# Kernel optimization log

Hardware: AMD Instinct MI355X
Metric: run time of the kernel (lower is better)

Reference implementation:

```python
import jax, jax.numpy as jnp
import numpy as np
import math

B, T, H, W = 32, 256, 16, 16
NE, NH, NL = 768, 12, 8
DH = NE // NH
SEQ_LEN = 1024


def _ln(x, g, b, eps=1e-5):
    m = jnp.mean(x, axis=-1, keepdims=True)
    v = jnp.mean((x - m) ** 2, axis=-1, keepdims=True)
    return (x - m) * jax.lax.rsqrt(v + eps) * g + b


def setup_inputs() -> dict:
    key = jax.random.key(0)
    ks = jax.random.split(key, 24)
    s = 0.02
    d = {}
    d["img_feat"] = jax.random.normal(ks[0], (B, 2048, H, W), jnp.float32)
    d["vm_patches"] = jax.random.normal(ks[1], (B, T, 256), jnp.float32)
    d["fm_patches"] = jax.random.normal(ks[2], (B, T, 256), jnp.float32)
    # token embedding params
    d["conv_w"] = jax.random.normal(ks[3], (NE // 2, 2048, 3, 3), jnp.float32) * s
    d["conv_b"] = jnp.zeros((NE // 2,), jnp.float32)
    d["vm_w"] = jax.random.normal(ks[4], (256, NE // 4), jnp.float32) * s
    d["vm_b"] = jnp.zeros((NE // 4,), jnp.float32)
    d["fm_w"] = jax.random.normal(ks[5], (256, NE // 4), jnp.float32) * s
    d["fm_b"] = jnp.zeros((NE // 4,), jnp.float32)
    d["pos_emb"] = jax.random.normal(ks[6], (SEQ_LEN, NE), jnp.float32) * s
    # stacked per-layer block params (leading dim NL, consumed by lax.scan)
    d["ln1_g"] = jnp.ones((NL, NE), jnp.float32)
    d["ln1_b"] = jnp.zeros((NL, NE), jnp.float32)
    d["Wq"] = jax.random.normal(ks[7], (NL, NE, NE), jnp.float32) * s
    d["bq"] = jnp.zeros((NL, NE), jnp.float32)
    d["Wk"] = jax.random.normal(ks[8], (NL, NE, NE), jnp.float32) * s
    d["bk"] = jnp.zeros((NL, NE), jnp.float32)
    d["Wv"] = jax.random.normal(ks[9], (NL, NE, NE), jnp.float32) * s
    d["bv"] = jnp.zeros((NL, NE), jnp.float32)
    d["Wo"] = jax.random.normal(ks[10], (NL, NE, NE), jnp.float32) * s
    d["bo"] = jnp.zeros((NL, NE), jnp.float32)
    d["ln2_g"] = jnp.ones((NL, NE), jnp.float32)
    d["ln2_b"] = jnp.zeros((NL, NE), jnp.float32)
    d["W1"] = jax.random.normal(ks[11], (NL, NE, 4 * NE), jnp.float32) * s
    d["b1"] = jnp.zeros((NL, 4 * NE), jnp.float32)
    d["W2"] = jax.random.normal(ks[12], (NL, 4 * NE, NE), jnp.float32) * s
    d["b2"] = jnp.zeros((NL, NE), jnp.float32)
    # prediction head params
    d["dec_ln1_g"] = jnp.ones((NE,), jnp.float32)
    d["dec_ln1_b"] = jnp.zeros((NE,), jnp.float32)
    d["dec_w"] = jax.random.normal(ks[13], (NE, NE), jnp.float32) * s
    d["dec_b"] = jnp.zeros((NE,), jnp.float32)
    d["dec_ln2_g"] = jnp.ones((NE,), jnp.float32)
    d["dec_ln2_b"] = jnp.zeros((NE,), jnp.float32)
    d["head_w"] = jax.random.normal(ks[14], (NE, 256), jnp.float32) * s
    d["head_b"] = jnp.zeros((256,), jnp.float32)
    return d


def reference(img_feat, vm_patches, fm_patches, conv_w, conv_b, vm_w, vm_b, fm_w, fm_b,
              pos_emb, ln1_g, ln1_b, Wq, bq, Wk, bk, Wv, bv, Wo, bo, ln2_g, ln2_b,
              W1, b1, W2, b2, dec_ln1_g, dec_ln1_b, dec_w, dec_b, dec_ln2_g, dec_ln2_b,
              head_w, head_b):
    # conv token embed: [B,2048,H,W] -> [B, NE//2, H, W] -> [B, T, NE//2]
    i_emb = jax.lax.conv_general_dilated(
        img_feat, conv_w, (1, 1), "SAME",
        dimension_numbers=("NCHW", "OIHW", "NCHW")) + conv_b[None, :, None, None]
    i_emb = i_emb.reshape(B, NE // 2, T).transpose(0, 2, 1)
    vm_emb = vm_patches @ vm_w + vm_b  # [B,T,NE//4]
    fm_emb = fm_patches @ fm_w + fm_b  # [B,T,NE//4]
    x = jnp.concatenate([i_emb, vm_emb, fm_emb], axis=2) + pos_emb[:T][None]  # [B,T,NE]

    scale = 1.0 / math.sqrt(DH)

    def block(x, p):
        g1, bb1_, wq, bq_, wk, bk_, wv, bv_, wo, bo_, g2, bb2_, w1, bm1, w2, bm2 = p
        h = _ln(x, g1, bb1_)
        q = (h @ wq + bq_).reshape(B, T, NH, DH)
        k = (h @ wk + bk_).reshape(B, T, NH, DH)
        v = (h @ wv + bv_).reshape(B, T, NH, DH)
        # mask in the original forward is hard-coded all-ones -> no masking
        att = jax.nn.softmax(jnp.einsum('bthd,bshd->bhts', q, k) * scale, axis=-1)
        y = jnp.einsum('bhts,bshd->bthd', att, v).reshape(B, T, NE)
        x = x + y @ wo + bo_
        h2 = _ln(x, g2, bb2_)
        x = x + jax.nn.gelu(h2 @ w1 + bm1, approximate=False) @ w2 + bm2
        return x, None

    x, _ = jax.lax.scan(block, x, (ln1_g, ln1_b, Wq, bq, Wk, bk, Wv, bv, Wo, bo,
                                   ln2_g, ln2_b, W1, b1, W2, b2))

    # Transformer_Prediction head
    x = _ln(x, dec_ln1_g, dec_ln1_b)
    x = jax.nn.gelu(x @ dec_w + dec_b, approximate=False)
    x = _ln(x, dec_ln2_g, dec_ln2_b)
    return x @ head_w + head_b  # [B,T,256]
```

## Files before the change

### kernel.cpp

```cpp
#include <hip/hip_runtime.h>
#include <stdint.h>

typedef short short8 __attribute__((ext_vector_type(8)));
typedef float v4f __attribute__((ext_vector_type(4)));

#define EPI_BF16    0
#define EPI_GELU    1
#define EPI_XPOS    3
#define EPI_ATOM    5
#define EPI_ATOMOUT 6

__device__ __forceinline__ uint16_t f2bf(float f) {
  uint32_t u = __float_as_uint(f);
  u += 0x7fffu + ((u >> 16) & 1u);
  return (uint16_t)(u >> 16);
}
__device__ __forceinline__ float bf2f(uint16_t h) {
  return __uint_as_float(((uint32_t)h) << 16);
}
__device__ __forceinline__ float gelu_f(float v) {
  return 0.5f * v * (1.f + erff(v * 0.70710678118654752f));
}
__device__ __forceinline__ void gld16(const uint16_t* g, uint16_t* l) {
  __builtin_amdgcn_global_load_lds(
      (const __attribute__((address_space(1))) void*)g,
      (__attribute__((address_space(3))) void*)l, 16, 0, 0);
}

struct TDesc {
  const float* src;
  uint16_t* dst;
  int K, N, batch;
  long long sstride, dstride;
  int tilesK, tilesN;
  long long tileStart;
};
struct TTable {
  TDesc d[12];
  int nd;
  long long totalTiles;
};

__global__ __launch_bounds__(256) void transpose_convert_kernel(TTable tt) {
  __shared__ float tile[32][33];
  const int tid = threadIdx.x;
  for (long long t = blockIdx.x; t < tt.totalTiles; t += gridDim.x) {
    int di = 0;
    while (di + 1 < tt.nd && t >= tt.d[di + 1].tileStart) di++;
    const TDesc d = tt.d[di];
    long long loc = t - d.tileStart;
    int perB = d.tilesK * d.tilesN;
    int bi = (int)(loc / perB);
    int r = (int)(loc % perB);
    int tk = r / d.tilesN, tn = r % d.tilesN;
    const float* src = d.src + (long long)bi * d.sstride;
    uint16_t* dst = d.dst + (long long)bi * d.dstride;
    int k0 = tk * 32, n0 = tn * 32;
#pragma unroll
    for (int p = 0; p < 4; p++) {
      int i = (tid >> 5) + p * 8;
      int k = k0 + i, n = n0 + (tid & 31);
      float v = 0.f;
      if (k < d.K && n < d.N) v = src[(long long)k * d.N + n];
      tile[i][tid & 31] = v;
    }
    __syncthreads();
#pragma unroll
    for (int p = 0; p < 4; p++) {
      int i = (tid >> 5) + p * 8;
      int n = n0 + i, k = k0 + (tid & 31);
      if (n < d.N && k < d.K) dst[(long long)n * d.K + k] = f2bf(tile[tid & 31][i]);
    }
    __syncthreads();
  }
}

__global__ __launch_bounds__(256) void conv_w_transpose(const float* __restrict__ src,
                                                        uint16_t* __restrict__ dst) {
  __shared__ float lds[2304];
  const int n = blockIdx.y;
  const int c0 = blockIdx.x * 256;
  const float* s = src + (size_t)n * 18432 + (size_t)c0 * 9;
  for (int j = threadIdx.x; j < 2304; j += 256) lds[j] = s[j];
  __syncthreads();
#pragma unroll
  for (int tap = 0; tap < 9; tap++)
    dst[(size_t)n * 18432 + tap * 2048 + c0 + threadIdx.x] =
        f2bf(lds[threadIdx.x * 9 + tap]);
}

__global__ __launch_bounds__(256) void img_pad_kernel(const float* __restrict__ img,
                                                      uint16_t* __restrict__ imgp) {
  __shared__ float tile[64][65];
  const int tid = threadIdx.x;
  const int b = blockIdx.z, ict = blockIdx.y, xyt = blockIdx.x;
  const int ic0 = ict * 64, xy0 = xyt * 64;
  const float* src = img + ((size_t)b * 2048 + ic0) * 256 + xy0;
#pragma unroll
  for (int p = 0; p < 16; p++) {
    int i = (tid >> 6) + p * 4;
    int j = tid & 63;
    tile[i][j] = src[(size_t)i * 256 + j];
  }
  __syncthreads();
#pragma unroll
  for (int p = 0; p < 16; p++) {
    int j = (tid >> 6) + p * 4;
    int i = tid & 63;
    int xy = xy0 + j;
    int y = xy >> 4, x = xy & 15;
    imgp[(((size_t)b * 18 + y + 1) * 18 + (x + 1)) * 2048 + ic0 + i] = f2bf(tile[i][j]);
  }
}

__global__ __launch_bounds__(256) void prep_kernel(const float* __restrict__ bq,
                                                   const float* __restrict__ bk,
                                                   const float* __restrict__ bv,
                                                   float* __restrict__ bqkv,
                                                   const float* __restrict__ vm,
                                                   const float* __restrict__ fm,
                                                   uint16_t* __restrict__ vmb,
                                                   uint16_t* __restrict__ fmb) {
  int idx = blockIdx.x * 256 + threadIdx.x;
  if (idx < 2097152) {
    vmb[idx] = f2bf(vm[idx]);
    fmb[idx] = f2bf(fm[idx]);
  }
  if (idx < 18432) {
    int l = idx / 2304, c = idx % 2304;
    float v = (c < 768) ? bq[l * 768 + c]
                        : ((c < 1536) ? bk[l * 768 + c - 768] : bv[l * 768 + c - 1536]);
    bqkv[idx] = v;
  }
}

__global__ __launch_bounds__(256) void xinit_kernel(const float* __restrict__ convb,
                                                    const float* __restrict__ pos,
                                                    float* __restrict__ x) {
  int idx = blockIdx.x * 256 + threadIdx.x;
  if (idx >= 8192 * 384) return;
  int m = idx / 384, n = idx % 384;
  x[(size_t)m * 768 + n] = convb[n] + pos[(size_t)(m & 255) * 768 + n];
}

template <int BF16IN>
__global__ __launch_bounds__(256) void ln_kernel(const void* __restrict__ inv,
                                                 const float* __restrict__ g,
                                                 const float* __restrict__ bta,
                                                 uint16_t* __restrict__ out) {
  const int row = blockIdx.x;
  const int tid = threadIdx.x;
  const float* inf = (const float*)inv;
  const uint16_t* inb = (const uint16_t*)inv;
  const size_t base = (size_t)row * 768;
  float v[3];
#pragma unroll
  for (int i = 0; i < 3; i++) {
    int c = tid + i * 256;
    v[i] = BF16IN ? bf2f(inb[base + c]) : inf[base + c];
  }
  float s = v[0] + v[1] + v[2];
  float s2 = v[0] * v[0] + v[1] * v[1] + v[2] * v[2];
#pragma unroll
  for (int d = 1; d < 64; d <<= 1) {
    s += __shfl_xor(s, d, 64);
    s2 += __shfl_xor(s2, d, 64);
  }
  __shared__ float ps[4], ps2[4];
  int wave = tid >> 6, lane = tid & 63;
  if (lane == 0) { ps[wave] = s; ps2[wave] = s2; }
  __syncthreads();
  s = ps[0] + ps[1] + ps[2] + ps[3];
  s2 = ps2[0] + ps2[1] + ps2[2] + ps2[3];
  float mean = s * (1.f / 768.f);
  float var = s2 * (1.f / 768.f) - mean * mean;
  float rs = rsqrtf(var + 1e-5f);
#pragma unroll
  for (int i = 0; i < 3; i++) {
    int c = tid + i * 256;
    out[base + c] = f2bf((v[i] - mean) * rs * g[c] + bta[c]);
  }
}

template <int AMODE, int EPI>
__global__ __launch_bounds__(256, 4) void gemm_kernel(
    const uint16_t* __restrict__ A, const uint16_t* __restrict__ Bt,
    const float* __restrict__ bias, int N, int K,
    float* xout,
    const float* __restrict__ pos, int colOff,
    uint16_t* __restrict__ outb, float* __restrict__ outf, int ldc) {
  __shared__ uint16_t ldsA[8192];
  __shared__ uint16_t ldsB[4096];
  const int tid = threadIdx.x;
  const int lane = tid & 63, wave = tid >> 6;
  const int l15 = lane & 15, q8 = (lane >> 4) << 3;
  const int row0 = blockIdx.x * 128, col0 = blockIdx.y * 64;
  const int kPer = K / (int)gridDim.z;
  const int kbeg = kPer * (int)blockIdx.z;
  const int wm = wave & 1, wn = wave >> 1;

  const uint16_t* srcP[6];
  uint16_t* dstP[6];
#pragma unroll
  for (int c = 0; c < 6; c++) {
    int j = wave * 6 + c;
    if (j < 16) {
      int mt8 = j >> 1, ks = j & 1;
      int m = row0 + mt8 * 16 + l15;
      srcP[c] = A + (size_t)m * K + ks * 32 + q8;
      dstP[c] = &ldsA[j * 512];
    } else {
      int fb = j - 16;
      int nt = fb >> 1, ks = fb & 1;
      int n = col0 + nt * 16 + l15;
      srcP[c] = Bt + (size_t)n * K + ks * 32 + q8;
      dstP[c] = &ldsB[fb * 512];
    }
  }

  v4f acc[4][2];
#pragma unroll
  for (int i = 0; i < 4; i++)
#pragma unroll
    for (int j = 0; j < 2; j++) acc[i][j] = (v4f){0.f, 0.f, 0.f, 0.f};

  for (int k0 = kbeg; k0 < kbeg + kPer; k0 += 64) {
    __syncthreads();
#pragma unroll
    for (int c = 0; c < 6; c++) gld16(srcP[c] + (size_t)k0, dstP[c]);
    __syncthreads();
#pragma unroll
    for (int ks = 0; ks < 2; ks++) {
      short8 af[4], bfr[2];
#pragma unroll
      for (int mt = 0; mt < 4; mt++)
        af[mt] = *(const short8*)&ldsA[(((wm * 4 + mt) * 2) + ks) * 512 + lane * 8];
#pragma unroll
      for (int nt = 0; nt < 2; nt++)
        bfr[nt] = *(const short8*)&ldsB[(((wn * 2 + nt) * 2) + ks) * 512 + lane * 8];
#pragma unroll
      for (int mt = 0; mt < 4; mt++)
#pragma unroll
        for (int nt = 0; nt < 2; nt++)
          acc[mt][nt] =
              __builtin_amdgcn_mfma_f32_16x16x32_bf16(af[mt], bfr[nt], acc[mt][nt], 0, 0, 0);
    }
  }

#pragma unroll
  for (int mt = 0; mt < 4; mt++) {
    int mbase = row0 + wm * 64 + mt * 16 + ((lane >> 4) << 2);
#pragma unroll
    for (int nt = 0; nt < 2; nt++) {
      int n = col0 + wn * 32 + nt * 16 + l15;
      float bv;
      if (EPI == EPI_ATOM)
        bv = (bias != nullptr && blockIdx.z == 0) ? bias[n] : 0.f;
      else if (EPI == EPI_ATOMOUT)
        bv = (blockIdx.z == 0) ? bias[n] : 0.f;
      else
        bv = bias[n];
      v4f a = acc[mt][nt];
#pragma unroll
      for (int r = 0; r < 4; r++) {
        int m = mbase + r;
        float v = a[r] + bv;
        if (EPI == EPI_BF16) {
          outb[(size_t)m * ldc + n] = f2bf(v);
        } else if (EPI == EPI_GELU) {
          outb[(size_t)m * ldc + n] = f2bf(gelu_f(v));
        } else if (EPI == EPI_XPOS) {
          xout[(size_t)m * 768 + colOff + n] = v + pos[(size_t)(m & 255) * 768 + colOff + n];
        } else if (EPI == EPI_ATOM) {
          atomicAdd(&xout[(size_t)m * 768 + colOff + n], v);
        } else if (EPI == EPI_ATOMOUT) {
          atomicAdd(&outf[(size_t)m * ldc + n], v);
        }
      }
    }
  }
}

template <int EPI>
__global__ __launch_bounds__(256, 2) void gemm128_kernel(
    const uint16_t* __restrict__ A, const uint16_t* __restrict__ Bt,
    const float* __restrict__ bias, int N, int K,
    float* xout,
    uint16_t* __restrict__ outb, float* __restrict__ outf, int ldc) {
  __shared__ uint16_t lds[2][16384];
  const int tid = threadIdx.x;
  const int lane = tid & 63, wave = tid >> 6;
  const int l15 = lane & 15, q8 = (lane >> 4) << 3;
  const int row0 = blockIdx.x * 128, col0 = blockIdx.y * 128;
  const int kPer = K / (int)gridDim.z;
  const int kbeg = kPer * (int)blockIdx.z;
  const int nt = kPer >> 6;
  const int wm = wave & 1, wn = wave >> 1;

  const uint16_t* srcP[8];
  int off[8];
#pragma unroll
  for (int c = 0; c < 8; c++) {
    int j = wave * 8 + c;
    if (j < 16) {
      int mt8 = j >> 1, ks = j & 1;
      int m = row0 + mt8 * 16 + l15;
      srcP[c] = A + (size_t)m * K + kbeg + ks * 32 + q8;
      off[c] = j * 512;
    } else {
      int fb = j - 16;
      int nt16 = fb >> 1, ks = fb & 1;
      int n = col0 + nt16 * 16 + l15;
      srcP[c] = Bt + (size_t)n * K + kbeg + ks * 32 + q8;
      off[c] = 8192 + fb * 512;
    }
  }

  auto STAGE = [&](int t) {
    size_t ko = (size_t)(t * 64);
    uint16_t* lb = &lds[t & 1][0];
#pragma unroll
    for (int c = 0; c < 8; c++) gld16(srcP[c] + ko, lb + off[c]);
  };

  v4f acc[4][4];
#pragma unroll
  for (int i = 0; i < 4; i++)
#pragma unroll
    for (int j = 0; j < 4; j++) acc[i][j] = (v4f){0.f, 0.f, 0.f, 0.f};

  STAGE(0);
  if (nt > 1) STAGE(1);

  for (int t = 0; t < nt; t++) {
    if (t + 1 < nt)
      asm volatile("s_waitcnt vmcnt(8)" ::: "memory");
    else
      asm volatile("s_waitcnt vmcnt(0)" ::: "memory");
    __builtin_amdgcn_s_barrier();

    const uint16_t* lb = &lds[t & 1][0];
#pragma unroll
    for (int ks = 0; ks < 2; ks++) {
      short8 af[4], bfr[4];
#pragma unroll
      for (int mt = 0; mt < 4; mt++)
        af[mt] = *(const short8*)&lb[(((wm * 4 + mt) * 2) + ks) * 512 + lane * 8];
#pragma unroll
      for (int nt2 = 0; nt2 < 4; nt2++)
        bfr[nt2] = *(const short8*)&lb[8192 + (((wn * 4 + nt2) * 2) + ks) * 512 + lane * 8];
#pragma unroll
      for (int mt = 0; mt < 4; mt++)
#pragma unroll
        for (int nt2 = 0; nt2 < 4; nt2++)
          acc[mt][nt2] =
              __builtin_amdgcn_mfma_f32_16x16x32_bf16(af[mt], bfr[nt2], acc[mt][nt2], 0, 0, 0);
    }

    __builtin_amdgcn_s_barrier();
    if (t + 2 < nt) STAGE(t + 2);
  }

#pragma unroll
  for (int mt = 0; mt < 4; mt++) {
    int mbase = row0 + wm * 64 + mt * 16 + ((lane >> 4) << 2);
#pragma unroll
    for (int nt2 = 0; nt2 < 4; nt2++) {
      int n = col0 + wn * 64 + nt2 * 16 + l15;
      float bv;
      if (EPI == EPI_ATOMOUT)
        bv = (blockIdx.z == 0) ? bias[n] : 0.f;
      else
        bv = bias[n];
      v4f a = acc[mt][nt2];
#pragma unroll
      for (int r = 0; r < 4; r++) {
        int m = mbase + r;
        float v = a[r] + bv;
        if (EPI == EPI_BF16) {
          outb[(size_t)m * ldc + n] = f2bf(v);
        } else if (EPI == EPI_GELU) {
          outb[(size_t)m * ldc + n] = f2bf(gelu_f(v));
        } else if (EPI == EPI_ATOMOUT) {
          atomicAdd(&outf[(size_t)m * ldc + n], v);
        }
      }
    }
  }
}

template <int AMODE, int EPI>
__global__ __launch_bounds__(512, 2) void gemm256_kernel(
    const uint16_t* __restrict__ A, const uint16_t* __restrict__ Bt,
    const float* __restrict__ bias, int N, int K,
    float* xout, uint16_t* __restrict__ outb, float* __restrict__ outf, int ldc) {
  extern __shared__ uint16_t lds[];
  const int tid = threadIdx.x;
  const int lane = tid & 63, wave = tid >> 6;
  const int l15 = lane & 15, q8 = (lane >> 4) << 3;

  const int nwg = (int)(gridDim.x * gridDim.y);
  const int lin = (int)(blockIdx.y * gridDim.x + blockIdx.x);
  const int swz = (lin & 7) * (nwg >> 3) + (lin >> 3);
  const int bx = swz % (int)gridDim.x, by = swz / (int)gridDim.x;

  const int row0 = bx * 256, col0 = by * 256;
  const int kPer = K / (int)gridDim.z;
  const int kbeg = kPer * (int)blockIdx.z;
  const int nt = kPer >> 6;
  const int wm = wave >> 2, wn = wave & 3;

  const uint16_t* src[4][2];
  int ldsoff[4][2];
#pragma unroll
  for (int c = 0; c < 2; c++) {
    int sub = wave * 2 + c;
    int hf = sub >> 1, ks = sub & 1;
    int kin = ks * 32 + q8;
    int m0 = row0 + hf * 16 + l15;
    int m1 = m0 + 128;
    if (AMODE == 0) {
      src[0][c] = A + (size_t)m0 * K + kin;
      src[3][c] = A + (size_t)m1 * K + kin;
    } else {
      int b0_ = m0 >> 8, y0_ = (m0 >> 4) & 15, x0_ = m0 & 15;
      src[0][c] = A + ((size_t)((b0_ * 18 + y0_) * 18 + x0_)) * 2048 + kin;
      int b1_ = m1 >> 8, y1_ = (m1 >> 4) & 15, x1_ = m1 & 15;
      src[3][c] = A + ((size_t)((b1_ * 18 + y1_) * 18 + x1_)) * 2048 + kin;
    }
    src[1][c] = Bt + (size_t)(col0 + hf * 16 + l15) * K + kin;
    src[2][c] = Bt + (size_t)(col0 + 128 + hf * 16 + l15) * K + kin;
    ldsoff[0][c] = sub * 512;
    ldsoff[3][c] = (16 + sub) * 512;
    ldsoff[1][c] = 16384 + sub * 512;
    ldsoff[2][c] = 16384 + (16 + sub) * 512;
  }

#define STAGEH(TT, Q)                                                          \
  do {                                                                         \
    int t_ = (TT);                                                             \
    if (t_ < nt) {                                                             \
      int k0_ = kbeg + t_ * 64;                                                \
      size_t o_;                                                               \
      if (AMODE == 1 && ((Q) == 0 || (Q) == 3)) {                              \
        int kq_ = k0_ >> 11;                                                   \
        int ky_ = (kq_ >= 6) ? 2 : ((kq_ >= 3) ? 1 : 0);                       \
        int kx_ = kq_ - ky_ * 3;                                               \
        o_ = (size_t)((ky_ * 18 + kx_) * 2048) + (size_t)(k0_ & 2047);         \
      } else {                                                                 \
        o_ = (size_t)k0_;                                                      \
      }                                                                        \
      uint16_t* lb_ = &lds[(t_ & 1) * 32768];                                  \
      gld16(src[Q][0] + o_, lb_ + ldsoff[Q][0]);                               \
      gld16(src[Q][1] + o_, lb_ + ldsoff[Q][1]);                               \
    }                                                                          \
  } while (0)

  v4f acc[8][4];
#pragma unroll
  for (int i = 0; i < 8; i++)
#pragma unroll
    for (int j = 0; j < 4; j++) acc[i][j] = (v4f){0.f, 0.f, 0.f, 0.f};

  STAGEH(0, 0); STAGEH(0, 1); STAGEH(0, 2); STAGEH(0, 3);
  STAGEH(1, 1); STAGEH(1, 0);
  asm volatile("s_waitcnt vmcnt(4)" ::: "memory");
  __builtin_amdgcn_s_barrier();

  short8 a_[4][2], aN[4][2], b0_[2][2], b1_[2][2];

#pragma unroll
  for (int mt = 0; mt < 4; mt++)
#pragma unroll
    for (int ks = 0; ks < 2; ks++)
      aN[mt][ks] = *(const short8*)&lds[((wm * 8 + mt) * 2 + ks) * 512 + lane * 8];

  for (int t = 0; t < nt; t++) {
    const int bufo = (t & 1) * 32768;

#pragma unroll
    for (int nl = 0; nl < 2; nl++)
#pragma unroll
      for (int ks = 0; ks < 2; ks++)
        b0_[nl][ks] =
            *(const short8*)&lds[bufo + 16384 + ((wn * 4 + nl) * 2 + ks) * 512 + lane * 8];
#pragma unroll
    for (int nl = 0; nl < 2; nl++)
#pragma unroll
      for (int ks = 0; ks < 2; ks++)
        b1_[nl][ks] =
            *(const short8*)&lds[bufo + 16384 + ((wn * 4 + 2 + nl) * 2 + ks) * 512 + lane * 8];
    STAGEH(t + 1, 2);
    __builtin_amdgcn_s_barrier();
    __builtin_amdgcn_s_setprio(1);
#pragma unroll
    for (int mt = 0; mt < 4; mt++)
#pragma unroll
      for (int nl = 0; nl < 2; nl++)
#pragma unroll
        for (int ks = 0; ks < 2; ks++)
          acc[mt][nl] =
              __builtin_amdgcn_mfma_f32_16x16x32_bf16(aN[mt][ks], b0_[nl][ks], acc[mt][nl], 0, 0, 0);
    __builtin_amdgcn_s_setprio(0);
    __builtin_amdgcn_s_barrier();

#pragma unroll
    for (int mt = 0; mt < 4; mt++)
#pragma unroll
      for (int ks = 0; ks < 2; ks++)
        a_[mt][ks] =
            *(const short8*)&lds[bufo + ((wm * 8 + 4 + mt) * 2 + ks) * 512 + lane * 8];
    STAGEH(t + 1, 3);
    __builtin_amdgcn_s_barrier();
    __builtin_amdgcn_s_setprio(1);
#pragma unroll
    for (int mt = 0; mt < 4; mt++)
#pragma unroll
      for (int nl = 0; nl < 2; nl++)
#pragma unroll
        for (int ks = 0; ks < 2; ks++)
          acc[mt][2 + nl] =
              __builtin_amdgcn_mfma_f32_16x16x32_bf16(aN[mt][ks], b1_[nl][ks], acc[mt][2 + nl], 0, 0, 0);
    __builtin_amdgcn_s_setprio(0);
    __builtin_amdgcn_s_barrier();

    STAGEH(t + 2, 1);
    __builtin_amdgcn_s_barrier();
    __builtin_amdgcn_s_setprio(1);
#pragma unroll
    for (int mt = 0; mt < 4; mt++)
#pragma unroll
      for (int nl = 0; nl < 2; nl++)
#pragma unroll
        for (int ks = 0; ks < 2; ks++)
          acc[4 + mt][2 + nl] =
              __builtin_amdgcn_mfma_f32_16x16x32_bf16(a_[mt][ks], b1_[nl][ks], acc[4 + mt][2 + nl], 0, 0, 0);
    __builtin_amdgcn_s_setprio(0);
    __builtin_amdgcn_s_barrier();

    STAGEH(t + 2, 0);
    if (t < nt - 1) {
      if (t == nt - 2)
        asm volatile("s_waitcnt vmcnt(0)" ::: "memory");
      else
        asm volatile("s_waitcnt vmcnt(4)" ::: "memory");
    }
    __builtin_amdgcn_s_barrier();
    if (t + 1 < nt) {
      const int bufn = ((t + 1) & 1) * 32768;
#pragma unroll
      for (int mt = 0; mt < 4; mt++)
#pragma unroll
        for (int ks = 0; ks < 2; ks++)
          aN[mt][ks] =
              *(const short8*)&lds[bufn + ((wm * 8 + mt) * 2 + ks) * 512 + lane * 8];
    }
    __builtin_amdgcn_s_setprio(1);
#pragma unroll
    for (int mt = 0; mt < 4; mt++)
#pragma unroll
      for (int nl = 0; nl < 2; nl++)
#pragma unroll
        for (int ks = 0; ks < 2; ks++)
          acc[4 + mt][nl] =
              __builtin_amdgcn_mfma_f32_16x16x32_bf16(a_[mt][ks], b0_[nl][ks], acc[4 + mt][nl], 0, 0, 0);
    __builtin_amdgcn_s_setprio(0);
    __builtin_amdgcn_s_barrier();
  }
#undef STAGEH

#pragma unroll
  for (int mt = 0; mt < 8; mt++) {
    int mbase = row0 + wm * 128 + mt * 16 + ((lane >> 4) << 2);
#pragma unroll
    for (int nl = 0; nl < 4; nl++) {
      int n = col0 + wn * 64 + nl * 16 + l15;
      float bv;
      if (EPI == EPI_ATOM)
        bv = (bias != nullptr && blockIdx.z == 0) ? bias[n] : 0.f;
      else
        bv = bias[n];
      v4f a = acc[mt][nl];
#pragma unroll
      for (int r = 0; r < 4; r++) {
        int m = mbase + r;
        float v = a[r] + bv;
        if (EPI == EPI_BF16) {
          outb[(size_t)m * ldc + n] = f2bf(v);
        } else if (EPI == EPI_GELU) {
          outb[(size_t)m * ldc + n] = f2bf(gelu_f(v));
        } else if (EPI == EPI_ATOM) {
          atomicAdd(&xout[(size_t)m * 768 + n], v);
        }
      }
    }
  }
}

__global__ __launch_bounds__(256) void attn_kernel(const uint16_t* __restrict__ qkv,
                                                   uint16_t* __restrict__ y) {
  __shared__ uint16_t KP[18432];
  __shared__ uint16_t Vt[64 * 264];
  uint16_t* Kl = KP;
  uint16_t(*Pl)[16 * 264] = (uint16_t(*)[16 * 264])KP;
  const int tid = threadIdx.x, lane = tid & 63, wave = tid >> 6;
  const int qc = blockIdx.x, h = blockIdx.y, b = blockIdx.z;
  const uint16_t* base = qkv + (size_t)b * 256 * 2304;
  const uint16_t* kb = base + 768 + h * 64;
  const uint16_t* vb = base + 1536 + h * 64;

#pragma unroll
  for (int i = 0; i < 8; i++) {
    int c = i * 256 + tid;
    int t = c >> 3, dh = (c & 7) * 8;
    uint4 d = *(const uint4*)(kb + (size_t)t * 2304 + dh);
    *(uint4*)&Kl[t * 72 + dh] = d;
  }
#pragma unroll
  for (int i = 0; i < 8; i++) {
    int c = i * 256 + tid;
    int t = c >> 3, dh = (c & 7) * 8;
    uint4 d = *(const uint4*)(vb + (size_t)t * 2304 + dh);
    const uint16_t* e = (const uint16_t*)&d;
#pragma unroll
    for (int j = 0; j < 8; j++) Vt[(dh + j) * 264 + t] = e[j];
  }
  __syncthreads();

  const int t0 = qc * 64 + wave * 16;
  const uint16_t* qb = base + h * 64;
  const int l15 = lane & 15, q4 = (lane >> 4) << 3;
  short8 aq0 = *(const short8*)(qb + (size_t)(t0 + l15) * 2304 + q4);
  short8 aq1 = *(const short8*)(qb + (size_t)(t0 + l15) * 2304 + 32 + q4);

  v4f s[16];
#pragma unroll
  for (int jt = 0; jt < 16; jt++) {
    short8 b0 = *(const short8*)&Kl[(jt * 16 + l15) * 72 + q4];
    short8 b1 = *(const short8*)&Kl[(jt * 16 + l15) * 72 + 32 + q4];
    v4f z = (v4f){0.f, 0.f, 0.f, 0.f};
    z = __builtin_amdgcn_mfma_f32_16x16x32_bf16(aq0, b0, z, 0, 0, 0);
    s[jt] = __builtin_amdgcn_mfma_f32_16x16x32_bf16(aq1, b1, z, 0, 0, 0);
  }

  float mx[4], sm[4];
#pragma unroll
  for (int r = 0; r < 4; r++) mx[r] = -1e30f;
#pragma unroll
  for (int jt = 0; jt < 16; jt++)
#pragma unroll
    for (int r = 0; r < 4; r++) {
      float v = s[jt][r] * 0.125f;
      s[jt][r] = v;
      mx[r] = fmaxf(mx[r], v);
    }
#pragma unroll
  for (int r = 0; r < 4; r++) {
#pragma unroll
    for (int d = 1; d < 16; d <<= 1) mx[r] = fmaxf(mx[r], __shfl_xor(mx[r], d, 64));
    sm[r] = 0.f;
  }
#pragma unroll
  for (int jt = 0; jt < 16; jt++)
#pragma unroll
    for (int r = 0; r < 4; r++) {
      float e = __expf(s[jt][r] - mx[r]);
      s[jt][r] = e;
      sm[r] += e;
    }
#pragma unroll
  for (int r = 0; r < 4; r++) {
#pragma unroll
    for (int d = 1; d < 16; d <<= 1) sm[r] += __shfl_xor(sm[r], d, 64);
    sm[r] = 1.f / sm[r];
  }

  __syncthreads();

  const int rbase = (lane >> 4) << 2;
#pragma unroll
  for (int jt = 0; jt < 16; jt++)
#pragma unroll
    for (int r = 0; r < 4; r++)
      Pl[wave][(rbase + r) * 264 + jt * 16 + l15] = f2bf(s[jt][r] * sm[r]);
  __syncthreads();

  v4f o[4];
#pragma unroll
  for (int nt = 0; nt < 4; nt++) o[nt] = (v4f){0.f, 0.f, 0.f, 0.f};
#pragma unroll
  for (int ks = 0; ks < 8; ks++) {
    short8 ap = *(const short8*)&Pl[wave][l15 * 264 + ks * 32 + q4];
#pragma unroll
    for (int nt = 0; nt < 4; nt++) {
      short8 bv8 = *(const short8*)&Vt[(nt * 16 + l15) * 264 + ks * 32 + q4];
      o[nt] = __builtin_amdgcn_mfma_f32_16x16x32_bf16(ap, bv8, o[nt], 0, 0, 0);
    }
  }
#pragma unroll
  for (int nt = 0; nt < 4; nt++)
#pragma unroll
    for (int r = 0; r < 4; r++)
      y[(size_t)(b * 256 + t0 + rbase + r) * 768 + h * 64 + nt * 16 + l15] = f2bf(o[nt][r]);
}

extern "C" void kernel_launch(void* const* d_in, const int* in_sizes, int n_in,
                              void* d_out, int out_size, void* d_ws, size_t ws_size,
                              hipStream_t stream) {
  const float* img   = (const float*)d_in[0];
  const float* vmp   = (const float*)d_in[1];
  const float* fmp   = (const float*)d_in[2];
  const float* convw = (const float*)d_in[3];
  const float* convb = (const float*)d_in[4];
  const float* vmw   = (const float*)d_in[5];
  const float* vmb_  = (const float*)d_in[6];
  const float* fmw   = (const float*)d_in[7];
  const float* fmb_  = (const float*)d_in[8];
  const float* pos   = (const float*)d_in[9];
  const float* ln1g  = (const float*)d_in[10];
  const float* ln1b  = (const float*)d_in[11];
  const float* Wq    = (const float*)d_in[12];
  const float* bq    = (const float*)d_in[13];
  const float* Wk    = (const float*)d_in[14];
  const float* bk    = (const float*)d_in[15];
  const float* Wv    = (const float*)d_in[16];
  const float* bv    = (const float*)d_in[17];
  const float* Wo    = (const float*)d_in[18];
  const float* bo    = (const float*)d_in[19];
  const float* ln2g  = (const float*)d_in[20];
  const float* ln2b  = (const float*)d_in[21];
  const float* W1    = (const float*)d_in[22];
  const float* b1    = (const float*)d_in[23];
  const float* W2    = (const float*)d_in[24];
  const float* b2    = (const float*)d_in[25];
  const float* dln1g = (const float*)d_in[26];
  const float* dln1b = (const float*)d_in[27];
  const float* decw  = (const float*)d_in[28];
  const float* decb  = (const float*)d_in[29];
  const float* dln2g = (const float*)d_in[30];
  const float* dln2b = (const float*)d_in[31];
  const float* headw = (const float*)d_in[32];
  const float* headb = (const float*)d_in[33];
  float* out = (float*)d_out;

  char* wsb = (char*)d_ws;
  size_t off = 0;
  auto alloc = [&](size_t nbytes) -> void* {
    off = (off + 255) & ~(size_t)255;
    void* p = wsb + off;
    off += nbytes;
    return p;
  };
  uint16_t* WtQKV  = (uint16_t*)alloc(8ull * 2304 * 768 * 2);
  uint16_t* WtO    = (uint16_t*)alloc(8ull * 768 * 768 * 2);
  uint16_t* Wt1    = (uint16_t*)alloc(8ull * 3072 * 768 * 2);
  uint16_t* Wt2    = (uint16_t*)alloc(8ull * 768 * 3072 * 2);
  uint16_t* WtConv = (uint16_t*)alloc(512ull * 9 * 2048 * 2);
  uint16_t* WtVm   = (uint16_t*)alloc(192ull * 256 * 2);
  uint16_t* WtFm   = (uint16_t*)alloc(192ull * 256 * 2);
  uint16_t* WtDec  = (uint16_t*)alloc(768ull * 768 * 2);
  uint16_t* WtHead = (uint16_t*)alloc(256ull * 768 * 2);
  uint16_t* imgp   = (uint16_t*)alloc(32ull * 18 * 18 * 2048 * 2);
  uint16_t* vmb    = (uint16_t*)alloc(8192ull * 256 * 2);
  uint16_t* fmb    = (uint16_t*)alloc(8192ull * 256 * 2);
  float*    bqkv   = (float*)alloc(8ull * 2304 * 4);
  float*    x      = (float*)alloc(8192ull * 768 * 4);
  uint16_t* hbuf   = (uint16_t*)alloc(8192ull * 768 * 2);
  uint16_t* qkvb   = (uint16_t*)alloc(8192ull * 2304 * 2);
  uint16_t* ybuf   = (uint16_t*)alloc(8192ull * 768 * 2);
  uint16_t* ubuf   = (uint16_t*)alloc(8192ull * 3072 * 2);
  uint16_t* u2buf  = (uint16_t*)alloc(8192ull * 768 * 2);
  if (off > ws_size) return;

  hipMemsetAsync(imgp, 0, 32ull * 18 * 18 * 2048 * 2, stream);
  hipMemsetAsync(WtConv, 0, 512ull * 9 * 2048 * 2, stream);
  hipMemsetAsync(out, 0, (size_t)out_size * 4, stream);

  hipFuncSetAttribute((const void*)gemm256_kernel<1, EPI_ATOM>,
                      hipFuncAttributeMaxDynamicSharedMemorySize, 131072);
  hipFuncSetAttribute((const void*)gemm256_kernel<0, EPI_ATOM>,
                      hipFuncAttributeMaxDynamicSharedMemorySize, 131072);
  hipFuncSetAttribute((const void*)gemm256_kernel<0, EPI_BF16>,
                      hipFuncAttributeMaxDynamicSharedMemorySize, 131072);
  hipFuncSetAttribute((const void*)gemm256_kernel<0, EPI_GELU>,
                      hipFuncAttributeMaxDynamicSharedMemorySize, 131072);

  TTable tt;
  int nd = 0;
  long long tiles = 0;
  auto addT = [&](const float* src, uint16_t* dst, int K, int N, int batch,
                  long long sstr, long long dstr) {
    TDesc& d = tt.d[nd];
    d.src = src; d.dst = dst; d.K = K; d.N = N; d.batch = batch;
    d.sstride = sstr; d.dstride = dstr;
    d.tilesK = (K + 31) / 32; d.tilesN = (N + 31) / 32;
    d.tileStart = tiles;
    tiles += (long long)d.tilesK * d.tilesN * batch;
    nd++;
  };
  addT(Wq, WtQKV,           768, 768, 8, 589824, 1769472);
  addT(Wk, WtQKV + 589824,  768, 768, 8, 589824, 1769472);
  addT(Wv, WtQKV + 1179648, 768, 768, 8, 589824, 1769472);
  addT(Wo, WtO,             768, 768, 8, 589824, 589824);
  addT(W1, Wt1,             768, 3072, 8, 2359296, 2359296);
  addT(W2, Wt2,             3072, 768, 8, 2359296, 2359296);
  addT(vmw, WtVm,           256, 192, 1, 0, 0);
  addT(fmw, WtFm,           256, 192, 1, 0, 0);
  addT(decw, WtDec,         768, 768, 1, 0, 0);
  addT(headw, WtHead,       768, 256, 1, 0, 0);
  tt.nd = nd;
  tt.totalTiles = tiles;

  transpose_convert_kernel<<<(int)tiles, 256, 0, stream>>>(tt);
  conv_w_transpose<<<dim3(8, 384), 256, 0, stream>>>(convw, WtConv);
  img_pad_kernel<<<dim3(4, 32, 32), 256, 0, stream>>>(img, imgp);
  prep_kernel<<<8192, 256, 0, stream>>>(bq, bk, bv, bqkv, vmp, fmp, vmb, fmb);
  xinit_kernel<<<12288, 256, 0, stream>>>(convb, pos, x);

  gemm256_kernel<1, EPI_ATOM><<<dim3(32, 2, 4), 512, 131072, stream>>>(
      imgp, WtConv, nullptr, 512, 18432, x, nullptr, nullptr, 0);
  gemm_kernel<0, EPI_XPOS><<<dim3(64, 3), 256, 0, stream>>>(
      vmb, WtVm, vmb_, 192, 256, x, pos, 384, nullptr, nullptr, 0);
  gemm_kernel<0, EPI_XPOS><<<dim3(64, 3), 256, 0, stream>>>(
      fmb, WtFm, fmb_, 192, 256, x, pos, 576, nullptr, nullptr, 0);

  for (int l = 0; l < 8; l++) {
    ln_kernel<0><<<8192, 256, 0, stream>>>(x, ln1g + l * 768, ln1b + l * 768, hbuf);
    gemm256_kernel<0, EPI_BF16><<<dim3(32, 9), 512, 131072, stream>>>(
        hbuf, WtQKV + (size_t)l * 1769472, bqkv + l * 2304, 2304, 768,
        nullptr, qkvb, nullptr, 2304);
    attn_kernel<<<dim3(4, 12, 32), 256, 0, stream>>>(qkvb, ybuf);
    gemm256_kernel<0, EPI_ATOM><<<dim3(32, 3, 2), 512, 131072, stream>>>(
        ybuf, WtO + (size_t)l * 589824, bo + l * 768, 768, 768,
        x, nullptr, nullptr, 0);
    ln_kernel<0><<<8192, 256, 0, stream>>>(x, ln2g + l * 768, ln2b + l * 768, hbuf);
    gemm256_kernel<0, EPI_GELU><<<dim3(32, 12), 512, 131072, stream>>>(
        hbuf, Wt1 + (size_t)l * 2359296, b1 + l * 3072, 3072, 768,
        nullptr, ubuf, nullptr, 3072);
    gemm256_kernel<0, EPI_ATOM><<<dim3(32, 3, 2), 512, 131072, stream>>>(
        ubuf, Wt2 + (size_t)l * 2359296, b2 + l * 768, 768, 3072,
        x, nullptr, nullptr, 0);
  }

  ln_kernel<0><<<8192, 256, 0, stream>>>(x, dln1g, dln1b, hbuf);
  gemm128_kernel<EPI_GELU><<<dim3(64, 6), 256, 0, stream>>>(
      hbuf, WtDec, decb, 768, 768, nullptr, u2buf, nullptr, 768);
  ln_kernel<1><<<8192, 256, 0, stream>>>(u2buf, dln2g, dln2b, hbuf);
  gemm128_kernel<EPI_ATOMOUT><<<dim3(64, 2, 2), 256, 0, stream>>>(
      hbuf, WtHead, headb, 256, 768, nullptr, nullptr, out, 256);
}
```

Measured before the change: 3.317 ms.

## Add 256x384-tile GEMM kernel for transformer layers, swizzle attention V LDS

Adds a 12-wave gemm384 kernel with 256x384 output tiles, double-buffered global_load_lds staging and interleaved MFMA phases. It replaces the 256x256 GEMM for the QKV, output-projection, MLP-up and MLP-down matmuls, with a larger split-K for the atomic epilogues. It also removes the workgroup-index swizzle from the remaining gemm256 path and XOR-swizzles the transposed V tile in attention to reduce LDS bank conflicts. Bigger tiles should cut operand reloads, at the cost of higher LDS and register pressure, fewer blocks, and more atomics from the deeper split-K.

```diff
diff --git a/kernel.cpp b/kernel.cpp
--- a/kernel.cpp
+++ b/kernel.cpp
@@ -398,13 +398,7 @@
   const int tid = threadIdx.x;
   const int lane = tid & 63, wave = tid >> 6;
   const int l15 = lane & 15, q8 = (lane >> 4) << 3;
-
-  const int nwg = (int)(gridDim.x * gridDim.y);
-  const int lin = (int)(blockIdx.y * gridDim.x + blockIdx.x);
-  const int swz = (lin & 7) * (nwg >> 3) + (lin >> 3);
-  const int bx = swz % (int)gridDim.x, by = swz / (int)gridDim.x;
-
-  const int row0 = bx * 256, col0 = by * 256;
+  const int row0 = blockIdx.x * 256, col0 = blockIdx.y * 256;
   const int kPer = K / (int)gridDim.z;
   const int kbeg = kPer * (int)blockIdx.z;
   const int nt = kPer >> 6;
@@ -597,6 +591,240 @@
   }
 }
 
+template <int EPI>
+__global__ __launch_bounds__(768, 3) void gemm384_kernel(
+    const uint16_t* __restrict__ A, const uint16_t* __restrict__ Bt,
+    const float* __restrict__ bias, int N, int K,
+    float* xout, uint16_t* __restrict__ outb, float* __restrict__ outf, int ldc) {
+  extern __shared__ uint16_t lds[];
+  const int tid = threadIdx.x;
+  const int lane = tid & 63, wave = tid >> 6;
+  const int l15 = lane & 15, q8 = (lane >> 4) << 3;
+  const int row0 = blockIdx.x * 256, col0 = blockIdx.y * 384;
+  const int kPer = K / (int)gridDim.z;
+  const int kbeg = kPer * (int)blockIdx.z;
+  const int nt = kPer >> 6;
+  const int wm = wave / 6, wn = wave % 6;
+
+  const uint16_t* sU0[2];
+  int oU0[2];
+  const uint16_t* sU3[2];
+  int oU3[2];
+  const uint16_t* sU1[2];
+  int oU1[2];
+  const uint16_t* sU2[2];
+  int oU2[2];
+  {
+    int kin0 = 0 * 32 + q8, kin1 = 1 * 32 + q8;
+    sU0[0] = A + (size_t)(row0 + wave * 16 + l15) * K + kin0;
+    sU0[1] = A + (size_t)(row0 + wave * 16 + l15) * K + kin1;
+    oU0[0] = (wave * 2 + 0) * 512;
+    oU0[1] = (wave * 2 + 1) * 512;
+    sU3[0] = A + (size_t)(row0 + (wave + 4) * 16 + l15) * K + kin0;
+    sU3[1] = A + (size_t)(row0 + (wave + 4) * 16 + l15) * K + kin1;
+    oU3[0] = ((wave + 4) * 2 + 0) * 512;
+    oU3[1] = ((wave + 4) * 2 + 1) * 512;
+    sU1[0] = Bt + (size_t)(col0 + wave * 16 + l15) * K + kin0;
+    sU1[1] = Bt + (size_t)(col0 + wave * 16 + l15) * K + kin1;
+    oU1[0] = 16384 + (wave * 2 + 0) * 512;
+    oU1[1] = 16384 + (wave * 2 + 1) * 512;
+    sU2[0] = Bt + (size_t)(col0 + 192 + wave * 16 + l15) * K + kin0;
+    sU2[1] = Bt + (size_t)(col0 + 192 + wave * 16 + l15) * K + kin1;
+    oU2[0] = 16384 + ((12 + wave) * 2 + 0) * 512;
+    oU2[1] = 16384 + ((12 + wave) * 2 + 1) * 512;
+  }
+
+#define ST_U0(TT)                                                              \
+  do {                                                                         \
+    int t_ = (TT);                                                             \
+    if (t_ < nt && wave < 8) {                                                 \
+      size_t o_ = (size_t)(kbeg + t_ * 64);                                    \
+      uint16_t* lb_ = &lds[(t_ & 1) * 40960];                                  \
+      gld16(sU0[0] + o_, lb_ + oU0[0]);                                        \
+      gld16(sU0[1] + o_, lb_ + oU0[1]);                                        \
+    }                                                                          \
+  } while (0)
+#define ST_U3(TT)                                                              \
+  do {                                                                         \
+    int t_ = (TT);                                                             \
+    if (t_ < nt && wave >= 4) {                                                \
+      size_t o_ = (size_t)(kbeg + t_ * 64);                                    \
+      uint16_t* lb_ = &lds[(t_ & 1) * 40960];                                  \
+      gld16(sU3[0] + o_, lb_ + oU3[0]);                                        \
+      gld16(sU3[1] + o_, lb_ + oU3[1]);                                        \
+    }                                                                          \
+  } while (0)
+#define ST_U1(TT)                                                              \
+  do {                                                                         \
+    int t_ = (TT);                                                             \
+    if (t_ < nt) {                                                             \
+      size_t o_ = (size_t)(kbeg + t_ * 64);                                    \
+      uint16_t* lb_ = &lds[(t_ & 1) * 40960];                                  \
+      gld16(sU1[0] + o_, lb_ + oU1[0]);                                        \
+      gld16(sU1[1] + o_, lb_ + oU1[1]);                                        \
+    }                                                                          \
+  } while (0)
+#define ST_U2(TT)                                                              \
+  do {                                                                         \
+    int t_ = (TT);                                                             \
+    if (t_ < nt) {                                                             \
+      size_t o_ = (size_t)(kbeg + t_ * 64);                                    \
+      uint16_t* lb_ = &lds[(t_ & 1) * 40960];                                  \
+      gld16(sU2[0] + o_, lb_ + oU2[0]);                                        \
+      gld16(sU2[1] + o_, lb_ + oU2[1]);                                        \
+    }                                                                          \
+  } while (0)
+
+  v4f acc[8][4];
+#pragma unroll
+  for (int i = 0; i < 8; i++)
+#pragma unroll
+    for (int j = 0; j < 4; j++) acc[i][j] = (v4f){0.f, 0.f, 0.f, 0.f};
+
+  ST_U0(0); ST_U1(0); ST_U2(0); ST_U3(0);
+  ST_U0(1); ST_U1(1);
+  if (wave < 8)
+    asm volatile("s_waitcnt vmcnt(4)" ::: "memory");
+  else
+    asm volatile("s_waitcnt vmcnt(2)" ::: "memory");
+  __builtin_amdgcn_s_barrier();
+
+  short8 a_[4][2], aN[4][2], b0_[2][2], b1_[2][2];
+
+#pragma unroll
+  for (int mt = 0; mt < 4; mt++)
+#pragma unroll
+    for (int ks = 0; ks < 2; ks++)
+      aN[mt][ks] = *(const short8*)&lds[((wm * 8 + mt) * 2 + ks) * 512 + lane * 8];
+
+  for (int t = 0; t < nt; t++) {
+    const int bufo = (t & 1) * 40960;
+
+#pragma unroll
+    for (int nl = 0; nl < 2; nl++)
+#pragma unroll
+      for (int ks = 0; ks < 2; ks++)
+        b0_[nl][ks] =
+            *(const short8*)&lds[bufo + 16384 + ((wn * 4 + nl) * 2 + ks) * 512 + lane * 8];
+#pragma unroll
+    for (int nl = 0; nl < 2; nl++)
+#pragma unroll
+      for (int ks = 0; ks < 2; ks++)
+        b1_[nl][ks] =
+            *(const short8*)&lds[bufo + 16384 + ((wn * 4 + 2 + nl) * 2 + ks) * 512 + lane * 8];
+    ST_U2(t + 1);
+    __builtin_amdgcn_s_barrier();
+    __builtin_amdgcn_s_setprio(1);
+#pragma unroll
+    for (int mt = 0; mt < 4; mt++)
+#pragma unroll
+      for (int nl = 0; nl < 2; nl++)
+#pragma unroll
+        for (int ks = 0; ks < 2; ks++)
+          acc[mt][nl] =
+              __builtin_amdgcn_mfma_f32_16x16x32_bf16(aN[mt][ks], b0_[nl][ks], acc[mt][nl], 0, 0, 0);
+    __builtin_amdgcn_s_setprio(0);
+    __builtin_amdgcn_s_barrier();
+
+#pragma unroll
+    for (int mt = 0; mt < 4; mt++)
+#pragma unroll
+      for (int ks = 0; ks < 2; ks++)
+        a_[mt][ks] =
+            *(const short8*)&lds[bufo + ((wm * 8 + 4 + mt) * 2 + ks) * 512 + lane * 8];
+    ST_U3(t + 1);
+    __builtin_amdgcn_s_barrier();
+    __builtin_amdgcn_s_setprio(1);
+#pragma unroll
+    for (int mt = 0; mt < 4; mt++)
+#pragma unroll
+      for (int nl = 0; nl < 2; nl++)
+#pragma unroll
+        for (int ks = 0; ks < 2; ks++)
+          acc[mt][2 + nl] =
+              __builtin_amdgcn_mfma_f32_16x16x32_bf16(aN[mt][ks], b1_[nl][ks], acc[mt][2 + nl], 0, 0, 0);
+    __builtin_amdgcn_s_setprio(0);
+    __builtin_amdgcn_s_barrier();
+
+    ST_U1(t + 2);
+    __builtin_amdgcn_s_barrier();
+    __builtin_amdgcn_s_setprio(1);
+#pragma unroll
+    for (int mt = 0; mt < 4; mt++)
+#pragma unroll
+      for (int nl = 0; nl < 2; nl++)
+#pragma unroll
+        for (int ks = 0; ks < 2; ks++)
+          acc[4 + mt][2 + nl] =
+              __builtin_amdgcn_mfma_f32_16x16x32_bf16(a_[mt][ks], b1_[nl][ks], acc[4 + mt][2 + nl], 0, 0, 0);
+    __builtin_amdgcn_s_setprio(0);
+    __builtin_amdgcn_s_barrier();
+
+    ST_U0(t + 2);
+    if (t < nt - 1) {
+      if (t == nt - 2) {
+        asm volatile("s_waitcnt vmcnt(0)" ::: "memory");
+      } else if (wave < 8) {
+        asm volatile("s_waitcnt vmcnt(4)" ::: "memory");
+      } else {
+        asm volatile("s_waitcnt vmcnt(2)" ::: "memory");
+      }
+    }
+    __builtin_amdgcn_s_barrier();
+    if (t + 1 < nt) {
+      const int bufn = ((t + 1) & 1) * 40960;
+#pragma unroll
+      for (int mt = 0; mt < 4; mt++)
+#pragma unroll
+        for (int ks = 0; ks < 2; ks++)
+          aN[mt][ks] =
+              *(const short8*)&lds[bufn + ((wm * 8 + mt) * 2 + ks) * 512 + lane * 8];
+    }
+    __builtin_amdgcn_s_setprio(1);
+#pragma unroll
+    for (int mt = 0; mt < 4; mt++)
+#pragma unroll
+      for (int nl = 0; nl < 2; nl++)
+#pragma unroll
+        for (int ks = 0; ks < 2; ks++)
+          acc[4 + mt][nl] =
+              __builtin_amdgcn_mfma_f32_16x16x32_bf16(a_[mt][ks], b0_[nl][ks], acc[4 + mt][nl], 0, 0, 0);
+    __builtin_amdgcn_s_setprio(0);
+    __builtin_amdgcn_s_barrier();
+  }
+#undef ST_U0
+#undef ST_U1
+#undef ST_U2
+#undef ST_U3
+
+#pragma unroll
+  for (int mt = 0; mt < 8; mt++) {
+    int mbase = row0 + wm * 128 + mt * 16 + ((lane >> 4) << 2);
+#pragma unroll
+    for (int nl = 0; nl < 4; nl++) {
+      int n = col0 + wn * 64 + nl * 16 + l15;
+      float bv;
+      if (EPI == EPI_ATOM)
+        bv = (bias != nullptr && blockIdx.z == 0) ? bias[n] : 0.f;
+      else
+        bv = bias[n];
+      v4f a = acc[mt][nl];
+#pragma unroll
+      for (int r = 0; r < 4; r++) {
+        int m = mbase + r;
+        float v = a[r] + bv;
+        if (EPI == EPI_BF16) {
+          outb[(size_t)m * ldc + n] = f2bf(v);
+        } else if (EPI == EPI_GELU) {
+          outb[(size_t)m * ldc + n] = f2bf(gelu_f(v));
+        } else if (EPI == EPI_ATOM) {
+          atomicAdd(&xout[(size_t)m * 768 + n], v);
+        }
+      }
+    }
+  }
+}
+
 __global__ __launch_bounds__(256) void attn_kernel(const uint16_t* __restrict__ qkv,
                                                    uint16_t* __restrict__ y) {
   __shared__ uint16_t KP[18432];
@@ -622,8 +850,9 @@
     int t = c >> 3, dh = (c & 7) * 8;
     uint4 d = *(const uint4*)(vb + (size_t)t * 2304 + dh);
     const uint16_t* e = (const uint16_t*)&d;
-#pragma unroll
-    for (int j = 0; j < 8; j++) Vt[(dh + j) * 264 + t] = e[j];
+    int tc = t ^ (((dh >> 3) & 7) << 3);
+#pragma unroll
+    for (int j = 0; j < 8; j++) Vt[(dh + j) * 264 + tc] = e[j];
   }
   __syncthreads();
 
@@ -693,7 +922,9 @@
     short8 ap = *(const short8*)&Pl[wave][l15 * 264 + ks * 32 + q4];
 #pragma unroll
     for (int nt = 0; nt < 4; nt++) {
-      short8 bv8 = *(const short8*)&Vt[(nt * 16 + l15) * 264 + ks * 32 + q4];
+      int row = nt * 16 + l15;
+      int col = (ks * 32 + q4) ^ (((row >> 3) & 7) << 3);
+      short8 bv8 = *(const short8*)&Vt[row * 264 + col];
       o[nt] = __builtin_amdgcn_mfma_f32_16x16x32_bf16(ap, bv8, o[nt], 0, 0, 0);
     }
   }
@@ -778,12 +1009,12 @@
 
   hipFuncSetAttribute((const void*)gemm256_kernel<1, EPI_ATOM>,
                       hipFuncAttributeMaxDynamicSharedMemorySize, 131072);
-  hipFuncSetAttribute((const void*)gemm256_kernel<0, EPI_ATOM>,
-                      hipFuncAttributeMaxDynamicSharedMemorySize, 131072);
-  hipFuncSetAttribute((const void*)gemm256_kernel<0, EPI_BF16>,
-                      hipFuncAttributeMaxDynamicSharedMemorySize, 131072);
-  hipFuncSetAttribute((const void*)gemm256_kernel<0, EPI_GELU>,
-                      hipFuncAttributeMaxDynamicSharedMemorySize, 131072);
+  hipFuncSetAttribute((const void*)gemm384_kernel<EPI_BF16>,
+                      hipFuncAttributeMaxDynamicSharedMemorySize, 163840);
+  hipFuncSetAttribute((const void*)gemm384_kernel<EPI_GELU>,
+                      hipFuncAttributeMaxDynamicSharedMemorySize, 163840);
+  hipFuncSetAttribute((const void*)gemm384_kernel<EPI_ATOM>,
+                      hipFuncAttributeMaxDynamicSharedMemorySize, 163840);
 
   TTable tt;
   int nd = 0;
@@ -826,18 +1057,18 @@
 
   for (int l = 0; l < 8; l++) {
     ln_kernel<0><<<8192, 256, 0, stream>>>(x, ln1g + l * 768, ln1b + l * 768, hbuf);
-    gemm256_kernel<0, EPI_BF16><<<dim3(32, 9), 512, 131072, stream>>>(
+    gemm384_kernel<EPI_BF16><<<dim3(32, 6), 768, 163840, stream>>>(
         hbuf, WtQKV + (size_t)l * 1769472, bqkv + l * 2304, 2304, 768,
         nullptr, qkvb, nullptr, 2304);
     attn_kernel<<<dim3(4, 12, 32), 256, 0, stream>>>(qkvb, ybuf);
-    gemm256_kernel<0, EPI_ATOM><<<dim3(32, 3, 2), 512, 131072, stream>>>(
+    gemm384_kernel<EPI_ATOM><<<dim3(32, 2, 4), 768, 163840, stream>>>(
         ybuf, WtO + (size_t)l * 589824, bo + l * 768, 768, 768,
         x, nullptr, nullptr, 0);
     ln_kernel<0><<<8192, 256, 0, stream>>>(x, ln2g + l * 768, ln2b + l * 768, hbuf);
-    gemm256_kernel<0, EPI_GELU><<<dim3(32, 12), 512, 131072, stream>>>(
+    gemm384_kernel<EPI_GELU><<<dim3(32, 8), 768, 163840, stream>>>(
         hbuf, Wt1 + (size_t)l * 2359296, b1 + l * 3072, 3072, 768,
         nullptr, ubuf, nullptr, 3072);
-    gemm256_kernel<0, EPI_ATOM><<<dim3(32, 3, 2), 512, 131072, stream>>>(
+    gemm384_kernel<EPI_ATOM><<<dim3(32, 2, 4), 768, 163840, stream>>>(
         ubuf, Wt2 + (size_t)l * 2359296, b2 + l * 768, 768, 3072,
         x, nullptr, nullptr, 0);
   }
```

Result: slower. 8.663 ms (+161.2%).

## Use wave-per-row layernorm, drop GEMM tile swizzle, XOR-swizzle attention V tile

Applied to the files above, without the earlier changes.

LayerNorm now handles one row per wavefront, four rows per block, which removes the shared-memory reduction and barrier. The gemm256 workgroup remapping swizzle is dropped in favour of a direct blockIdx mapping. The attention kernel's transposed V tile in LDS gets an XOR column swizzle, meant to cut bank conflicts on its transposed scalar stores and vector reads. Dropping the swizzle may reduce L2 reuse in the large GEMMs.

```diff
diff --git a/kernel.cpp b/kernel.cpp
--- a/kernel.cpp
+++ b/kernel.cpp
@@ -148,36 +148,34 @@
                                                  const float* __restrict__ g,
                                                  const float* __restrict__ bta,
                                                  uint16_t* __restrict__ out) {
-  const int row = blockIdx.x;
-  const int tid = threadIdx.x;
+  const int wave = threadIdx.x >> 6, lane = threadIdx.x & 63;
+  const int row = blockIdx.x * 4 + wave;
   const float* inf = (const float*)inv;
   const uint16_t* inb = (const uint16_t*)inv;
   const size_t base = (size_t)row * 768;
-  float v[3];
-#pragma unroll
-  for (int i = 0; i < 3; i++) {
-    int c = tid + i * 256;
+  float v[12];
+#pragma unroll
+  for (int i = 0; i < 12; i++) {
+    int c = lane + i * 64;
     v[i] = BF16IN ? bf2f(inb[base + c]) : inf[base + c];
   }
-  float s = v[0] + v[1] + v[2];
-  float s2 = v[0] * v[0] + v[1] * v[1] + v[2] * v[2];
+  float s = 0.f, s2 = 0.f;
+#pragma unroll
+  for (int i = 0; i < 12; i++) {
+    s += v[i];
+    s2 += v[i] * v[i];
+  }
 #pragma unroll
   for (int d = 1; d < 64; d <<= 1) {
     s += __shfl_xor(s, d, 64);
     s2 += __shfl_xor(s2, d, 64);
   }
-  __shared__ float ps[4], ps2[4];
-  int wave = tid >> 6, lane = tid & 63;
-  if (lane == 0) { ps[wave] = s; ps2[wave] = s2; }
-  __syncthreads();
-  s = ps[0] + ps[1] + ps[2] + ps[3];
-  s2 = ps2[0] + ps2[1] + ps2[2] + ps2[3];
   float mean = s * (1.f / 768.f);
   float var = s2 * (1.f / 768.f) - mean * mean;
   float rs = rsqrtf(var + 1e-5f);
 #pragma unroll
-  for (int i = 0; i < 3; i++) {
-    int c = tid + i * 256;
+  for (int i = 0; i < 12; i++) {
+    int c = lane + i * 64;
     out[base + c] = f2bf((v[i] - mean) * rs * g[c] + bta[c]);
   }
 }
@@ -398,13 +396,7 @@
   const int tid = threadIdx.x;
   const int lane = tid & 63, wave = tid >> 6;
   const int l15 = lane & 15, q8 = (lane >> 4) << 3;
-
-  const int nwg = (int)(gridDim.x * gridDim.y);
-  const int lin = (int)(blockIdx.y * gridDim.x + blockIdx.x);
-  const int swz = (lin & 7) * (nwg >> 3) + (lin >> 3);
-  const int bx = swz % (int)gridDim.x, by = swz / (int)gridDim.x;
-
-  const int row0 = bx * 256, col0 = by * 256;
+  const int row0 = blockIdx.x * 256, col0 = blockIdx.y * 256;
   const int kPer = K / (int)gridDim.z;
   const int kbeg = kPer * (int)blockIdx.z;
   const int nt = kPer >> 6;
@@ -622,8 +614,9 @@
     int t = c >> 3, dh = (c & 7) * 8;
     uint4 d = *(const uint4*)(vb + (size_t)t * 2304 + dh);
     const uint16_t* e = (const uint16_t*)&d;
-#pragma unroll
-    for (int j = 0; j < 8; j++) Vt[(dh + j) * 264 + t] = e[j];
+    int tc = t ^ (((dh >> 3) & 7) << 3);
+#pragma unroll
+    for (int j = 0; j < 8; j++) Vt[(dh + j) * 264 + tc] = e[j];
   }
   __syncthreads();
 
@@ -693,7 +686,9 @@
     short8 ap = *(const short8*)&Pl[wave][l15 * 264 + ks * 32 + q4];
 #pragma unroll
     for (int nt = 0; nt < 4; nt++) {
-      short8 bv8 = *(const short8*)&Vt[(nt * 16 + l15) * 264 + ks * 32 + q4];
+      int row = nt * 16 + l15;
+      int col = (ks * 32 + q4) ^ (((row >> 3) & 7) << 3);
+      short8 bv8 = *(const short8*)&Vt[row * 264 + col];
       o[nt] = __builtin_amdgcn_mfma_f32_16x16x32_bf16(ap, bv8, o[nt], 0, 0, 0);
     }
   }
@@ -825,7 +820,7 @@
       fmb, WtFm, fmb_, 192, 256, x, pos, 576, nullptr, nullptr, 0);
 
   for (int l = 0; l < 8; l++) {
-    ln_kernel<0><<<8192, 256, 0, stream>>>(x, ln1g + l * 768, ln1b + l * 768, hbuf);
+    ln_kernel<0><<<2048, 256, 0, stream>>>(x, ln1g + l * 768, ln1b + l * 768, hbuf);
     gemm256_kernel<0, EPI_BF16><<<dim3(32, 9), 512, 131072, stream>>>(
         hbuf, WtQKV + (size_t)l * 1769472, bqkv + l * 2304, 2304, 768,
         nullptr, qkvb, nullptr, 2304);
@@ -833,7 +828,7 @@
     gemm256_kernel<0, EPI_ATOM><<<dim3(32, 3, 2), 512, 131072, stream>>>(
         ybuf, WtO + (size_t)l * 589824, bo + l * 768, 768, 768,
         x, nullptr, nullptr, 0);
-    ln_kernel<0><<<8192, 256, 0, stream>>>(x, ln2g + l * 768, ln2b + l * 768, hbuf);
+    ln_kernel<0><<<2048, 256, 0, stream>>>(x, ln2g + l * 768, ln2b + l * 768, hbuf);
     gemm256_kernel<0, EPI_GELU><<<dim3(32, 12), 512, 131072, stream>>>(
         hbuf, Wt1 + (size_t)l * 2359296, b1 + l * 3072, 3072, 768,
         nullptr, ubuf, nullptr, 3072);
@@ -842,10 +837,10 @@
         x, nullptr, nullptr, 0);
   }
 
-  ln_kernel<0><<<8192, 256, 0, stream>>>(x, dln1g, dln1b, hbuf);
+  ln_kernel<0><<<2048, 256, 0, stream>>>(x, dln1g, dln1b, hbuf);
   gemm128_kernel<EPI_GELU><<<dim3(64, 6), 256, 0, stream>>>(
       hbuf, WtDec, decb, 768, 768, nullptr, u2buf, nullptr, 768);
-  ln_kernel<1><<<8192, 256, 0, stream>>>(u2buf, dln2g, dln2b, hbuf);
+  ln_kernel<1><<<2048, 256, 0, stream>>>(u2buf, dln2g, dln2b, hbuf);
   gemm128_kernel<EPI_ATOMOUT><<<dim3(64, 2, 2), 256, 0, stream>>>(
       hbuf, WtHead, headb, 256, 768, nullptr, nullptr, out, 256);
 }
```

Result: no change. 3.306 ms (-0.3%).
